# Performance work log

Measured on AMD Instinct MI355X. Metric: run time of the kernel, lower is better.

The kernel has to match this reference:

```python
import jax, jax.numpy as jnp
import numpy as np

SEQ, EMB, OUT = 8192, 1024, 128

def setup_inputs() -> dict:
    key = jax.random.key(0)
    k1, k2, k3, k4 = jax.random.split(key, 4)
    return {
        "x": jax.random.normal(k1, (SEQ, EMB), dtype=jnp.float32),
        "wquery": jax.random.normal(k2, (EMB, OUT), dtype=jnp.float32) * (2.0 / EMB) ** 0.5,
        "wkey": jax.random.normal(k3, (EMB, OUT), dtype=jnp.float32) * (2.0 / EMB) ** 0.5,
        "wvalue": jax.random.normal(k4, (EMB, OUT), dtype=jnp.float32) * (2.0 / EMB) ** 0.5,
    }

def reference(x, wquery, wkey, wvalue):
    # Single-head attention, mask=True branch (mask tensor is zeros -> no masking).
    q = x @ wquery   # [S, D]
    k = x @ wkey     # [S, D]
    v = x @ wvalue   # [S, D]
    scale = jnp.sqrt(jnp.asarray(q.shape[-1], dtype=q.dtype))
    a = (q @ k.T) / scale              # [S, S]
    p = jax.nn.softmax(a, axis=1)      # softmax over keys (dim=1 in torch)
    return p @ v                       # [S, D]
```

## Files before the change

### kernel.cpp

```cpp
#include <hip/hip_runtime.h>
#include <cstdint>
#include <cstddef>

#define SEQ 8192
#define EMB 1024
#define DH  128

typedef __bf16 bf16x8 __attribute__((ext_vector_type(8)));
typedef __bf16 bf16x2 __attribute__((ext_vector_type(2)));
typedef float  f32x4  __attribute__((ext_vector_type(4)));
typedef float  f32x16 __attribute__((ext_vector_type(16)));
typedef uint32_t u32x4 __attribute__((ext_vector_type(4)));
typedef unsigned short u16x8 __attribute__((ext_vector_type(8)));

static constexpr float QSCALE = (float)(1.4426950408889634 / 11.313708498984760);

__device__ __forceinline__ unsigned short f2bf(float f) {
  uint32_t u = __builtin_bit_cast(uint32_t, f);
  u += 0x7FFFu + ((u >> 16) & 1u);
  return (unsigned short)(u >> 16);
}
__device__ __forceinline__ float bf2f(unsigned short u) {
  return __builtin_bit_cast(float, (uint32_t)u << 16);
}

#define GLD_LDS16(gsrc, ldst) \
  __builtin_amdgcn_global_load_lds((__attribute__((address_space(1))) void*)(gsrc), \
                                   (__attribute__((address_space(3))) void*)(ldst), 16, 0, 0)

__global__ __launch_bounds__(256) void convert_kernel(
    const float* __restrict__ x,
    const float* __restrict__ wq, const float* __restrict__ wk, const float* __restrict__ wv,
    unsigned short* __restrict__ xb, unsigned short* __restrict__ wt)
{
  const int bid = blockIdx.x;
  const int t = threadIdx.x;
  if (bid < 2048) {
    size_t e = (size_t)bid * 4096 + (size_t)t * 16;
#pragma unroll
    for (int i = 0; i < 2; ++i) {
      float4 a = *reinterpret_cast<const float4*>(x + e + i * 8);
      float4 b = *reinterpret_cast<const float4*>(x + e + i * 8 + 4);
      u16x8 o = { f2bf(a.x), f2bf(a.y), f2bf(a.z), f2bf(a.w),
                  f2bf(b.x), f2bf(b.y), f2bf(b.z), f2bf(b.w) };
      *reinterpret_cast<u16x8*>(xb + e + i * 8) = o;
    }
  } else {
    const int which = (bid - 2048) >> 2;
    const int k = ((bid - 2048) & 3) * 256 + t;
    const float* w = (which == 0) ? wq : ((which == 1) ? wk : wv);
    const float scl = (which == 0) ? QSCALE : 1.0f;
#pragma unroll
    for (int n = 0; n < 128; n += 4) {
      float4 v = *reinterpret_cast<const float4*>(w + (size_t)k * DH + n);
      wt[((size_t)which * DH + n + 0) * EMB + k] = f2bf(v.x * scl);
      wt[((size_t)which * DH + n + 1) * EMB + k] = f2bf(v.y * scl);
      wt[((size_t)which * DH + n + 2) * EMB + k] = f2bf(v.z * scl);
      wt[((size_t)which * DH + n + 3) * EMB + k] = f2bf(v.w * scl);
    }
  }
}

__global__ __launch_bounds__(256) void qkv_gemm(
    const unsigned short* __restrict__ xb, const unsigned short* __restrict__ wt,
    unsigned short* __restrict__ qs, unsigned short* __restrict__ ks,
    unsigned short* __restrict__ vt)
{
  __shared__ char LDS[49152];
  char* A0 = LDS;
  char* B0 = LDS + 16384;
  unsigned short* T = (unsigned short*)LDS;

  const int t    = threadIdx.x;
  const int lane = t & 63;
  const int wid  = t >> 6;
  const int wr   = wid >> 1, wc = wid & 1;
  const int l31  = lane & 31;
  const int hi   = lane >> 5;
  const int row0 = blockIdx.x * 64;
  const int which = blockIdx.y;

  const char* xc  = (const char*)xb;
  const char* wtc = (const char*)(wt + (size_t)which * DH * EMB);

  f32x16 acc[2] = {};

  auto STAGE = [&](int buf, int k0) {
#pragma unroll
    for (int i = 0; i < 2; ++i) {
      int bidx = i * 4096 + t * 16;
      int row = bidx >> 7, off = bidx & 127;
      const char* src = xc + (size_t)(row0 + row) * (EMB * 2) + k0 * 2 + (off ^ ((row & 7) << 4));
      GLD_LDS16(src, A0 + buf * 8192 + i * 4096 + wid * 1024);
    }
#pragma unroll
    for (int i = 0; i < 4; ++i) {
      int bidx = i * 4096 + t * 16;
      int n = bidx >> 7, off = bidx & 127;
      const char* src = wtc + (size_t)n * (EMB * 2) + k0 * 2 + (off ^ ((n & 7) << 4));
      GLD_LDS16(src, B0 + buf * 16384 + i * 4096 + wid * 1024);
    }
  };

  STAGE(0, 0);
  int cur = 0;
  for (int it = 0; it < EMB / 64; ++it) {
    if (it + 1 < EMB / 64) {
      STAGE(cur ^ 1, (it + 1) * 64);
      asm volatile("s_waitcnt vmcnt(6)" ::: "memory");
    } else {
      asm volatile("s_waitcnt vmcnt(0)" ::: "memory");
    }
    __builtin_amdgcn_s_barrier();
    asm volatile("" ::: "memory");

    const char* Ab = A0 + cur * 8192;
    const char* Bb = B0 + cur * 16384;
    const int ar   = wr * 32 + l31;
    const int aswz = (l31 & 7) << 4;

    __builtin_amdgcn_s_setprio(1);
#pragma unroll
    for (int kk = 0; kk < 4; ++kk) {
      bf16x8 af = *reinterpret_cast<const bf16x8*>(Ab + ar * 128 + ((kk * 32 + hi * 16) ^ aswz));
#pragma unroll
      for (int nt = 0; nt < 2; ++nt) {
        const int n = wc * 64 + nt * 32 + l31;
        bf16x8 bf = *reinterpret_cast<const bf16x8*>(Bb + n * 128 + ((kk * 32 + hi * 16) ^ ((n & 7) << 4)));
        acc[nt] = __builtin_amdgcn_mfma_f32_32x32x16_bf16(af, bf, acc[nt], 0, 0, 0);
      }
    }
    __builtin_amdgcn_s_setprio(0);

    asm volatile("" ::: "memory");
    __builtin_amdgcn_s_barrier();
    asm volatile("" ::: "memory");
    cur ^= 1;
  }

  if (which < 2) {
    unsigned short* dst = (which == 0) ? qs : ks;
#pragma unroll
    for (int nt = 0; nt < 2; ++nt)
#pragma unroll
      for (int r = 0; r < 16; ++r) {
        int row = row0 + wr * 32 + (r & 3) + 8 * (r >> 2) + 4 * hi;
        dst[(size_t)row * DH + wc * 64 + nt * 32 + l31] = f2bf(acc[nt][r]);
      }
  } else {
    __syncthreads();
#pragma unroll
    for (int nt = 0; nt < 2; ++nt)
#pragma unroll
      for (int r = 0; r < 16; ++r) {
        int d  = wc * 64 + nt * 32 + l31;
        int rl = wr * 32 + (r & 3) + 8 * (r >> 2) + 4 * hi;
        T[d * 72 + rl] = f2bf(acc[nt][r]);
      }
    __syncthreads();
    const int d = t >> 1, half = t & 1;
#pragma unroll
    for (int i = 0; i < 4; ++i) {
      uint4 v = *reinterpret_cast<const uint4*>(&T[d * 72 + half * 32 + i * 8]);
      *reinterpret_cast<uint4*>(vt + (size_t)d * SEQ + row0 + half * 32 + i * 8) = v;
    }
  }
}

template <int NS>
__global__ __launch_bounds__(512, 2) void attn_kernel(
    const unsigned short* __restrict__ qs, const unsigned short* __restrict__ ks,
    const unsigned short* __restrict__ vt,
    unsigned short* __restrict__ Obf, float* __restrict__ ml)
{
  __shared__ unsigned short Ks[2][64 * 128];
  __shared__ unsigned short Vt[2][128 * 64];

  const int t    = threadIdx.x;
  const int lane = t & 63;
  const int wid  = t >> 6;
  const int l31  = lane & 31;
  const int hi   = lane >> 5;
  const int swz  = (lane & 7) << 4;
  const int q0   = blockIdx.x * 256 + wid * 32;
  const int sp   = blockIdx.y;

  bf16x8 qf[8];
  {
    const unsigned short* qp = qs + (size_t)(q0 + l31) * DH + hi * 8;
#pragma unroll
    for (int ds = 0; ds < 8; ++ds)
      qf[ds] = *reinterpret_cast<const bf16x8*>(qp + ds * 16);
  }

  float l = 0.f;
  f32x16 O[4] = {};

  const char* ksc = (const char*)ks;
  const char* vtc = (const char*)vt;
  char* ksl = (char*)&Ks[0][0];
  char* vtl = (char*)&Vt[0][0];

  constexpr int CHUNK = SEQ / NS;
  constexpr int NT = CHUNK / 64;
  const int kv_base = sp * CHUNK;

  auto KSTAGE = [&](int tile) {
    const int kv0 = kv_base + tile * 64;
#pragma unroll
    for (int rr = 0; rr < 2; ++rr) {
      int bidx = rr * 512 + t;
      int key = bidx >> 4, blk = bidx & 15;
      const char* src = ksc + (size_t)(kv0 + key) * 256 + ((blk * 16) ^ ((key & 7) << 4));
      GLD_LDS16(src, ksl + (tile & 1) * 16384 + rr * 8192 + wid * 1024);
    }
  };
  auto VSTAGE = [&](int tile) {
    const int kv0 = kv_base + tile * 64;
#pragma unroll
    for (int rr = 0; rr < 2; ++rr) {
      int bidx = rr * 512 + t;
      int d = bidx >> 3, kb = bidx & 7;
      const char* src = vtc + (size_t)d * (SEQ * 2) + (size_t)kv0 * 2 + ((kb * 16) ^ ((d & 7) << 4));
      GLD_LDS16(src, vtl + (tile & 1) * 16384 + rr * 8192 + wid * 1024);
    }
  };

  auto QKT = [&](f32x16& T0, f32x16& T1, int tile) {
    const char* kb = ksl + (tile & 1) * 16384;
    f32x16 z = {};
    T0 = z; T1 = z;
#pragma unroll
    for (int ds = 0; ds < 8; ++ds) {
      bf16x8 ka = *reinterpret_cast<const bf16x8*>(kb + l31 * 256 + ((ds * 32 + hi * 16) ^ swz));
      T0 = __builtin_amdgcn_mfma_f32_32x32x16_bf16(ka, qf[ds], T0, 0, 0, 0);
    }
#pragma unroll
    for (int ds = 0; ds < 8; ++ds) {
      bf16x8 ka = *reinterpret_cast<const bf16x8*>(kb + 8192 + l31 * 256 + ((ds * 32 + hi * 16) ^ swz));
      T1 = __builtin_amdgcn_mfma_f32_32x32x16_bf16(ka, qf[ds], T1, 0, 0, 0);
    }
  };

  auto build2 = [&](const f32x16& P, bf16x8* fr) {
    uint32_t c[8];
#pragma unroll
    for (int i = 0; i < 8; ++i) {
      bf16x2 b2; b2[0] = (__bf16)P[2 * i]; b2[1] = (__bf16)P[2 * i + 1];
      c[i] = __builtin_bit_cast(uint32_t, b2);
    }
    uint32_t r0 = __shfl_xor(c[0], 32, 64), r1 = __shfl_xor(c[1], 32, 64);
    uint32_t r2 = __shfl_xor(c[2], 32, 64), r3 = __shfl_xor(c[3], 32, 64);
    u32x4 w0;
    w0[0] = hi ? r2 : c[0];
    w0[1] = hi ? r3 : c[1];
    w0[2] = hi ? c[2] : r0;
    w0[3] = hi ? c[3] : r1;
    uint32_t r4 = __shfl_xor(c[4], 32, 64), r5 = __shfl_xor(c[5], 32, 64);
    uint32_t r6 = __shfl_xor(c[6], 32, 64), r7 = __shfl_xor(c[7], 32, 64);
    u32x4 w1;
    w1[0] = hi ? r6 : c[4];
    w1[1] = hi ? r7 : c[5];
    w1[2] = hi ? c[6] : r4;
    w1[3] = hi ? c[7] : r5;
    fr[0] = __builtin_bit_cast(bf16x8, w0);
    fr[1] = __builtin_bit_cast(bf16x8, w1);
  };

  auto BODY = [&](int it, f32x16& Sc0, f32x16& Sc1, f32x16& Sn0, f32x16& Sn1) {
    if (it + 2 < NT) KSTAGE(it + 2);
    if (it + 1 < NT) VSTAGE(it + 1);

    if (it + 1 < NT) {
      __builtin_amdgcn_s_setprio(1);
      QKT(Sn0, Sn1, it + 1);
      __builtin_amdgcn_s_setprio(0);
    }

    float sm[16];
#pragma unroll
    for (int r = 0; r < 16; ++r) {
      Sc0[r] = __builtin_amdgcn_exp2f(Sc0[r]);
      Sc1[r] = __builtin_amdgcn_exp2f(Sc1[r]);
      sm[r] = Sc0[r] + Sc1[r];
    }
#pragma unroll
    for (int st = 8; st >= 1; st >>= 1)
#pragma unroll
      for (int r = 0; r < st; ++r) sm[r] += sm[r + st];
    l += sm[0] + __shfl_xor(sm[0], 32, 64);

    bf16x8 pa[4];
    build2(Sc0, &pa[0]);
    build2(Sc1, &pa[2]);

    const char* vb0 = vtl + (it & 1) * 16384;
    __builtin_amdgcn_s_setprio(1);
#pragma unroll
    for (int ks4 = 0; ks4 < 4; ++ks4) {
#pragma unroll
      for (int nt = 0; nt < 4; ++nt) {
        const int d = nt * 32 + l31;
        bf16x8 vb = *reinterpret_cast<const bf16x8*>(vb0 + d * 128 + ((ks4 * 32 + hi * 16) ^ swz));
        O[nt] = __builtin_amdgcn_mfma_f32_32x32x16_bf16(pa[ks4], vb, O[nt], 0, 0, 0);
      }
    }
    __builtin_amdgcn_s_setprio(0);

    asm volatile("s_waitcnt vmcnt(0)" ::: "memory");
    __builtin_amdgcn_s_barrier();
    asm volatile("" ::: "memory");
  };

  KSTAGE(0); VSTAGE(0); KSTAGE(1);
  asm volatile("s_waitcnt vmcnt(0)" ::: "memory");
  __builtin_amdgcn_s_barrier();
  asm volatile("" ::: "memory");

  f32x16 Sa0, Sa1, Sb0, Sb1;
  QKT(Sa0, Sa1, 0);
  asm volatile("" ::: "memory");
  __builtin_amdgcn_s_barrier();
  asm volatile("" ::: "memory");

  for (int it = 0; it < NT; it += 2) {
    BODY(it,     Sa0, Sa1, Sb0, Sb1);
    BODY(it + 1, Sb0, Sb1, Sa0, Sa1);
  }

  const float linv = 1.0f / l;
  unsigned short* Obase = Obf + ((size_t)sp * SEQ + q0) * DH;
#pragma unroll
  for (int r = 0; r < 16; ++r) {
    const int row = (r & 3) + 8 * (r >> 2) + 4 * hi;
    const float li = __shfl(linv, row, 64);
#pragma unroll
    for (int nt = 0; nt < 4; ++nt)
      Obase[(size_t)row * DH + nt * 32 + l31] = f2bf(O[nt][r] * li);
  }
  if (lane < 32) {
    ml[(size_t)sp * (2 * SEQ) + q0 + lane]       = 0.0f;
    ml[(size_t)sp * (2 * SEQ) + SEQ + q0 + lane] = l;
  }
}

template <int NS>
__global__ __launch_bounds__(256) void combine_kernel(
    const unsigned short* __restrict__ Obf, const float* __restrict__ ml, float* __restrict__ out)
{
  const int idx = blockIdx.x * 256 + threadIdx.x;
  const int s = idx >> 4;
  const int c = (idx & 15) * 8;
  float mv[NS], lv[NS];
  float M = -__builtin_inff();
#pragma unroll
  for (int i = 0; i < NS; ++i) {
    mv[i] = ml[(size_t)i * (2 * SEQ) + s];
    lv[i] = ml[(size_t)i * (2 * SEQ) + SEQ + s];
    M = fmaxf(M, mv[i]);
  }
  float den = 0.f;
  float num[8] = {};
#pragma unroll
  for (int i = 0; i < NS; ++i) {
    float g = __builtin_amdgcn_exp2f(mv[i] - M) * lv[i];
    den += g;
    u16x8 o = *reinterpret_cast<const u16x8*>(&Obf[((size_t)i * SEQ + s) * DH + c]);
#pragma unroll
    for (int j = 0; j < 8; ++j) num[j] += g * bf2f(o[j]);
  }
  const float inv = 1.f / den;
  f32x4 r0, r1;
#pragma unroll
  for (int j = 0; j < 4; ++j) { r0[j] = num[j] * inv; r1[j] = num[j + 4] * inv; }
  *reinterpret_cast<f32x4*>(&out[(size_t)s * DH + c])     = r0;
  *reinterpret_cast<f32x4*>(&out[(size_t)s * DH + c + 4]) = r1;
}

extern "C" void kernel_launch(void* const* d_in, const int* in_sizes, int n_in,
                              void* d_out, int out_size, void* d_ws, size_t ws_size,
                              hipStream_t stream) {
  const float* x  = (const float*)d_in[0];
  const float* wq = (const float*)d_in[1];
  const float* wk = (const float*)d_in[2];
  const float* wv = (const float*)d_in[3];
  float* out = (float*)d_out;

  char* ws = (char*)d_ws;
  const size_t MB = 1024 * 1024;
  unsigned short* qs = (unsigned short*)(ws);
  unsigned short* ks = (unsigned short*)(ws + 2 * MB);
  unsigned short* vt = (unsigned short*)(ws + 4 * MB);
  unsigned short* wt = (unsigned short*)(ws + 6 * MB);
  unsigned short* xb = (unsigned short*)(ws + 6 * MB + 768 * 1024);

  convert_kernel<<<2048 + 12, 256, 0, stream>>>(x, wq, wk, wv, xb, wt);
  qkv_gemm<<<dim3(SEQ / 64, 3), 256, 0, stream>>>(xb, wt, qs, ks, vt);

  unsigned short* Obf = (unsigned short*)(ws + 6 * MB);
  const size_t need8 = 6 * MB + 8ull * SEQ * DH * 2 + 8ull * 2 * SEQ * 4;
  if (ws_size >= need8) {
    float* ml = (float*)(ws + 6 * MB + 8ull * SEQ * DH * 2);
    attn_kernel<8><<<dim3(SEQ / 256, 8), 512, 0, stream>>>(qs, ks, vt, Obf, ml);
    combine_kernel<8><<<SEQ * DH / 8 / 256, 256, 0, stream>>>(Obf, ml, out);
  } else {
    float* ml = (float*)(ws + 6 * MB + 4ull * SEQ * DH * 2);
    attn_kernel<4><<<dim3(SEQ / 256, 4), 512, 0, stream>>>(qs, ks, vt, Obf, ml);
    combine_kernel<4><<<SEQ * DH / 8 / 256, 256, 0, stream>>>(Obf, ml, out);
  }
}
```

Measured before the change: 81.56 us.

## Fuse x fp32-to-bf16 conversion into QKV GEMM A-tile staging

Drops the separate pass that converts x to bf16 in workspace. The QKV GEMM now loads fp32 x into registers, converts it, and writes it swizzled into LDS, software-pipelined two iterations ahead, while B still uses direct global-to-LDS loads. This removes a kernel pass and the bf16 round trip through memory. In exchange, each of the three projection grids reads the full fp32 x, and the A staging adds VGPR pressure and register-to-LDS stores inside the main loop.

```diff
diff --git a/kernel.cpp b/kernel.cpp
--- a/kernel.cpp
+++ b/kernel.cpp
@@ -29,40 +29,27 @@
                                    (__attribute__((address_space(3))) void*)(ldst), 16, 0, 0)
 
 __global__ __launch_bounds__(256) void convert_kernel(
-    const float* __restrict__ x,
     const float* __restrict__ wq, const float* __restrict__ wk, const float* __restrict__ wv,
-    unsigned short* __restrict__ xb, unsigned short* __restrict__ wt)
+    unsigned short* __restrict__ wt)
 {
   const int bid = blockIdx.x;
   const int t = threadIdx.x;
-  if (bid < 2048) {
-    size_t e = (size_t)bid * 4096 + (size_t)t * 16;
-#pragma unroll
-    for (int i = 0; i < 2; ++i) {
-      float4 a = *reinterpret_cast<const float4*>(x + e + i * 8);
-      float4 b = *reinterpret_cast<const float4*>(x + e + i * 8 + 4);
-      u16x8 o = { f2bf(a.x), f2bf(a.y), f2bf(a.z), f2bf(a.w),
-                  f2bf(b.x), f2bf(b.y), f2bf(b.z), f2bf(b.w) };
-      *reinterpret_cast<u16x8*>(xb + e + i * 8) = o;
-    }
-  } else {
-    const int which = (bid - 2048) >> 2;
-    const int k = ((bid - 2048) & 3) * 256 + t;
-    const float* w = (which == 0) ? wq : ((which == 1) ? wk : wv);
-    const float scl = (which == 0) ? QSCALE : 1.0f;
-#pragma unroll
-    for (int n = 0; n < 128; n += 4) {
-      float4 v = *reinterpret_cast<const float4*>(w + (size_t)k * DH + n);
-      wt[((size_t)which * DH + n + 0) * EMB + k] = f2bf(v.x * scl);
-      wt[((size_t)which * DH + n + 1) * EMB + k] = f2bf(v.y * scl);
-      wt[((size_t)which * DH + n + 2) * EMB + k] = f2bf(v.z * scl);
-      wt[((size_t)which * DH + n + 3) * EMB + k] = f2bf(v.w * scl);
-    }
+  const int which = bid >> 2;
+  const int k = (bid & 3) * 256 + t;
+  const float* w = (which == 0) ? wq : ((which == 1) ? wk : wv);
+  const float scl = (which == 0) ? QSCALE : 1.0f;
+#pragma unroll
+  for (int n = 0; n < 128; n += 4) {
+    float4 v = *reinterpret_cast<const float4*>(w + (size_t)k * DH + n);
+    wt[((size_t)which * DH + n + 0) * EMB + k] = f2bf(v.x * scl);
+    wt[((size_t)which * DH + n + 1) * EMB + k] = f2bf(v.y * scl);
+    wt[((size_t)which * DH + n + 2) * EMB + k] = f2bf(v.z * scl);
+    wt[((size_t)which * DH + n + 3) * EMB + k] = f2bf(v.w * scl);
   }
 }
 
 __global__ __launch_bounds__(256) void qkv_gemm(
-    const unsigned short* __restrict__ xb, const unsigned short* __restrict__ wt,
+    const float* __restrict__ x, const unsigned short* __restrict__ wt,
     unsigned short* __restrict__ qs, unsigned short* __restrict__ ks,
     unsigned short* __restrict__ vt)
 {
@@ -80,19 +67,35 @@
   const int row0 = blockIdx.x * 64;
   const int which = blockIdx.y;
 
-  const char* xc  = (const char*)xb;
   const char* wtc = (const char*)(wt + (size_t)which * DH * EMB);
 
+  const int arow = t >> 2;
+  const int aq   = t & 3;
+  const float* xrow = x + (size_t)(row0 + arow) * EMB + aq * 16;
+  const int awz = (arow & 7) << 4;
+  const int aoff0 = (aq * 32 + 0)  ^ awz;
+  const int aoff1 = (aq * 32 + 16) ^ awz;
+
   f32x16 acc[2] = {};
-
-  auto STAGE = [&](int buf, int k0) {
-#pragma unroll
-    for (int i = 0; i < 2; ++i) {
-      int bidx = i * 4096 + t * 16;
-      int row = bidx >> 7, off = bidx & 127;
-      const char* src = xc + (size_t)(row0 + row) * (EMB * 2) + k0 * 2 + (off ^ ((row & 7) << 4));
-      GLD_LDS16(src, A0 + buf * 8192 + i * 4096 + wid * 1024);
-    }
+  float4 xa0, xa1, xa2, xa3;
+
+  auto ALOAD = [&](int k0) {
+    const float* s = xrow + k0;
+    xa0 = *reinterpret_cast<const float4*>(s + 0);
+    xa1 = *reinterpret_cast<const float4*>(s + 4);
+    xa2 = *reinterpret_cast<const float4*>(s + 8);
+    xa3 = *reinterpret_cast<const float4*>(s + 12);
+  };
+  auto AWRITE = [&](int buf) {
+    u16x8 h0 = { f2bf(xa0.x), f2bf(xa0.y), f2bf(xa0.z), f2bf(xa0.w),
+                 f2bf(xa1.x), f2bf(xa1.y), f2bf(xa1.z), f2bf(xa1.w) };
+    u16x8 h1 = { f2bf(xa2.x), f2bf(xa2.y), f2bf(xa2.z), f2bf(xa2.w),
+                 f2bf(xa3.x), f2bf(xa3.y), f2bf(xa3.z), f2bf(xa3.w) };
+    char* base = A0 + buf * 8192 + arow * 128;
+    *reinterpret_cast<u16x8*>(base + aoff0) = h0;
+    *reinterpret_cast<u16x8*>(base + aoff1) = h1;
+  };
+  auto BSTAGE = [&](int buf, int k0) {
 #pragma unroll
     for (int i = 0; i < 4; ++i) {
       int bidx = i * 4096 + t * 16;
@@ -102,17 +105,19 @@
     }
   };
 
-  STAGE(0, 0);
-  int cur = 0;
-  for (int it = 0; it < EMB / 64; ++it) {
-    if (it + 1 < EMB / 64) {
-      STAGE(cur ^ 1, (it + 1) * 64);
-      asm volatile("s_waitcnt vmcnt(6)" ::: "memory");
-    } else {
-      asm volatile("s_waitcnt vmcnt(0)" ::: "memory");
-    }
-    __builtin_amdgcn_s_barrier();
-    asm volatile("" ::: "memory");
+  constexpr int NI = EMB / 64;
+
+  ALOAD(0);
+  BSTAGE(0, 0);
+  AWRITE(0);
+  ALOAD(64);
+  asm volatile("s_waitcnt vmcnt(4) lgkmcnt(0)" ::: "memory");
+  __builtin_amdgcn_s_barrier();
+  asm volatile("" ::: "memory");
+
+  for (int it = 0; it < NI; ++it) {
+    const int cur = it & 1;
+    if (it + 1 < NI) BSTAGE(cur ^ 1, (it + 1) * 64);
 
     const char* Ab = A0 + cur * 8192;
     const char* Bb = B0 + cur * 16384;
@@ -132,10 +137,17 @@
     }
     __builtin_amdgcn_s_setprio(0);
 
-    asm volatile("" ::: "memory");
+    if (it + 1 < NI) {
+      AWRITE(cur ^ 1);
+      if (it + 2 < NI) {
+        ALOAD((it + 2) * 64);
+        asm volatile("s_waitcnt vmcnt(4) lgkmcnt(0)" ::: "memory");
+      } else {
+        asm volatile("s_waitcnt vmcnt(0) lgkmcnt(0)" ::: "memory");
+      }
+    }
     __builtin_amdgcn_s_barrier();
     asm volatile("" ::: "memory");
-    cur ^= 1;
   }
 
   if (which < 2) {
@@ -392,10 +404,9 @@
   unsigned short* ks = (unsigned short*)(ws + 2 * MB);
   unsigned short* vt = (unsigned short*)(ws + 4 * MB);
   unsigned short* wt = (unsigned short*)(ws + 6 * MB);
-  unsigned short* xb = (unsigned short*)(ws + 6 * MB + 768 * 1024);
-
-  convert_kernel<<<2048 + 12, 256, 0, stream>>>(x, wq, wk, wv, xb, wt);
-  qkv_gemm<<<dim3(SEQ / 64, 3), 256, 0, stream>>>(xb, wt, qs, ks, vt);
+
+  convert_kernel<<<12, 256, 0, stream>>>(wq, wk, wv, wt);
+  qkv_gemm<<<dim3(SEQ / 64, 3), 256, 0, stream>>>(x, wt, qs, ks, vt);
 
   unsigned short* Obf = (unsigned short*)(ws + 6 * MB);
   const size_t need8 = 6 * MB + 8ull * SEQ * DH * 2 + 8ull * 2 * SEQ * 4;
```

New measurement: 80.15 us (median of 2 runs). No clear change (-1.7%).
